# Performance work log

Hardware: AMD Instinct MI355X
Metric: run time of the kernel (lower is better)

The kernel has to match this reference:

```python
import jax, jax.numpy as jnp
import numpy as np

B, S, D, E, R, TOP_K = 4, 4096, 1024, 10, 4, 2
SCALING = 1.0 / R  # alpha / rank


def setup_inputs() -> dict:
    key = jax.random.key(0)
    ks = jax.random.split(key, 7)
    return {
        "x": jax.random.normal(ks[0], (B, S, D), dtype=jnp.float32),
        "W_base": jax.random.normal(ks[1], (D, D), dtype=jnp.float32) * (D ** -0.5),
        "b_base": jax.random.normal(ks[2], (D,), dtype=jnp.float32) * 0.02,
        "gate_W": jax.random.normal(ks[3], (E, D), dtype=jnp.float32) * (D ** -0.5),
        "gate_b": jax.random.normal(ks[4], (E,), dtype=jnp.float32) * 0.02,
        "lora_down": jax.random.normal(ks[5], (E, R, D), dtype=jnp.float32) * (D ** -0.5),
        "lora_up": jax.random.normal(ks[6], (E, D, R), dtype=jnp.float32) * (R ** -0.5),
    }


def reference(x, W_base, b_base, gate_W, gate_b, lora_down, lora_up):
    # Base (frozen) linear: [B,S,D]
    base_out = jnp.einsum("bsd,od->bso", x, W_base) + b_base

    # Top-k gating: logits [B,S,E] -> sparse softmax weights [B,S,E]
    logits = jnp.einsum("bsd,ed->bse", x, gate_W) + gate_b
    top_vals, top_idx = jax.lax.top_k(logits, TOP_K)          # [B,S,K]
    top_w = jax.nn.softmax(top_vals, axis=-1)                 # [B,S,K]
    # scatter top-k weights back to dense [B,S,E] (non-top-k are zero)
    weights = jnp.sum(top_w[..., None] * jax.nn.one_hot(top_idx, E, dtype=x.dtype), axis=-2)

    # All-expert LoRA (matches original loop); weight in rank space to avoid
    # materializing [B,S,E,D]: sum_e w_e * up_e(down_e(x)) * scaling
    h = jnp.einsum("bsd,erd->bser", x, lora_down)             # [B,S,E,R]
    h = h * weights[..., None]
    lora_out = jnp.einsum("bser,edr->bsd", h, lora_up) * SCALING

    return base_out + lora_out
```

## Files before the change

kernel.cpp:

```cpp
#include <hip/hip_runtime.h>
#include <hip/hip_bf16.h>
#include <cstdint>
#include <cstddef>

#define D_DIM 1024
#define E_NUM 10

typedef __attribute__((ext_vector_type(8))) short bf16x8;
typedef __attribute__((ext_vector_type(4))) float f32x4;
typedef unsigned short u16;
typedef unsigned int u32;

__device__ __forceinline__ u16 f2bf(float f) {
  union { float f; u32 u; } v; v.f = f;
  u32 r = v.u + 0x7fffu + ((v.u >> 16) & 1u);
  return (u16)(r >> 16);
}
__device__ __forceinline__ float bf2f(u16 u) {
  union { u32 u; float f; } v; v.u = ((u32)u) << 16; return v.f;
}
__device__ __forceinline__ float dot4(float4 a, float4 b) {
  return a.x * b.x + a.y * b.y + a.z * b.z + a.w * b.w;
}

__global__ void conv_w(const float* __restrict__ W, u16* __restrict__ Wb) {
  const int i = (blockIdx.x * 256 + threadIdx.x) * 8;
  float4 a = *(const float4*)(W + i);
  float4 b = *(const float4*)(W + i + 4);
  *(ushort4*)(Wb + i)     = make_ushort4(f2bf(a.x), f2bf(a.y), f2bf(a.z), f2bf(a.w));
  *(ushort4*)(Wb + i + 4) = make_ushort4(f2bf(b.x), f2bf(b.y), f2bf(b.z), f2bf(b.w));
}

__global__ void prep_ldb(const float* __restrict__ ld, u16* __restrict__ Bld) {
  const int r = blockIdx.x;
  for (int c = threadIdx.x; c < D_DIM; c += 256)
    Bld[r * D_DIM + c] = (r < 40) ? f2bf(ld[r * D_DIM + c]) : (u16)0;
}

__global__ __launch_bounds__(256)
void moe_prep_h(const float* __restrict__ x, const u16* __restrict__ Bld,
                float* __restrict__ h_all) {
  __shared__ u16 sX[4][16 * 64];
  __shared__ u16 sB[4][48 * 64];
  __shared__ float sP[4][3][16][17];

  const int tid = threadIdx.x, lane = tid & 63, w = tid >> 6;
  const int r0 = blockIdx.x * 16;
  const int kbase = w * 256;

  f32x4 acc[3] = {};

  float4 av[4];
#pragma unroll
  for (int i = 0; i < 2; ++i) {
    const int c = lane * 2 + i, row = c >> 3, kc = c & 7;
    const float* g = x + (size_t)(r0 + row) * D_DIM + kbase + kc * 8;
    av[i * 2]     = *(const float4*)g;
    av[i * 2 + 1] = *(const float4*)(g + 4);
  }

#pragma unroll 1
  for (int kt = 0; kt < 4; ++kt) {
    const int k0 = kbase + kt * 64;
#pragma unroll
    for (int i = 0; i < 6; ++i) {
      const int c = i * 64 + lane, row = c >> 3, kc = (c & 7) ^ (row & 7);
      __builtin_amdgcn_global_load_lds(
          (const __attribute__((address_space(1))) u32*)(Bld + (size_t)row * D_DIM + k0 + kc * 8),
          (__attribute__((address_space(3))) u32*)&sB[w][c * 8], 16, 0, 0);
    }
#pragma unroll
    for (int i = 0; i < 2; ++i) {
      const int c = lane * 2 + i, row = c >> 3, kc = c & 7;
      const float4 a = av[i * 2], b = av[i * 2 + 1];
      const int off = (row * 128 + kc * 16) ^ ((row & 7) << 4);
      *(ushort4*)((char*)sX[w] + off)     = make_ushort4(f2bf(a.x), f2bf(a.y), f2bf(a.z), f2bf(a.w));
      *(ushort4*)((char*)sX[w] + off + 8) = make_ushort4(f2bf(b.x), f2bf(b.y), f2bf(b.z), f2bf(b.w));
    }
    __syncthreads();
    if (kt < 3) {
#pragma unroll
      for (int i = 0; i < 2; ++i) {
        const int c = lane * 2 + i, row = c >> 3, kc = c & 7;
        const float* g = x + (size_t)(r0 + row) * D_DIM + (k0 + 64) + kc * 8;
        av[i * 2]     = *(const float4*)g;
        av[i * 2 + 1] = *(const float4*)(g + 4);
      }
    }
#pragma unroll
    for (int kk = 0; kk < 2; ++kk) {
      const int kb = kk * 64 + ((lane >> 4) * 16);
      const int rA = lane & 15;
      const bf16x8 a0 = *(const bf16x8*)((const char*)sX[w] + ((rA * 128 + kb) ^ ((rA & 7) << 4)));
#pragma unroll
      for (int cf = 0; cf < 3; ++cf) {
        const int rB = cf * 16 + (lane & 15);
        const bf16x8 q = *(const bf16x8*)((const char*)sB[w] + ((rB * 128 + kb) ^ ((rB & 7) << 4)));
        acc[cf] = __builtin_amdgcn_mfma_f32_16x16x32_bf16(a0, q, acc[cf], 0, 0, 0);
      }
    }
    __syncthreads();
  }

#pragma unroll
  for (int cf = 0; cf < 3; ++cf)
#pragma unroll
    for (int j = 0; j < 4; ++j)
      sP[w][cf][(lane >> 4) * 4 + j][lane & 15] = acc[cf][j];
  __syncthreads();

  const int row = tid >> 4, c16 = tid & 15;
#pragma unroll
  for (int cf = 0; cf < 3; ++cf) {
    const int col = cf * 16 + c16;
    if (col < 40) {
      const float s = sP[0][cf][row][c16] + sP[1][cf][row][c16] +
                      sP[2][cf][row][c16] + sP[3][cf][row][c16];
      h_all[(size_t)(r0 + row) * 40 + col] = s;
    }
  }
}

__global__ __launch_bounds__(256, 2)
void moe_gate(const float* __restrict__ x, const float* __restrict__ gW,
              const float* __restrict__ gb, const float* __restrict__ h_all,
              int* __restrict__ ids, float* __restrict__ cvals) {
  __shared__ float sgW[E_NUM * D_DIM];
  __shared__ float sgb[16];
  const int tid = threadIdx.x, lane = tid & 63, w = tid >> 6;
  for (int i = tid; i < E_NUM * D_DIM; i += 256) sgW[i] = gW[i];
  if (tid < E_NUM) sgb[tid] = gb[tid];
  __syncthreads();

  const int tb = blockIdx.x * 16 + w * 4;

  float4 xv[4][4];
#pragma unroll
  for (int tok = 0; tok < 4; ++tok)
#pragma unroll
    for (int j = 0; j < 4; ++j)
      xv[tok][j] = *(const float4*)(x + (size_t)(tb + tok) * D_DIM + j * 256 + lane * 4);

  float lg[4][E_NUM];
#pragma unroll
  for (int e = 0; e < E_NUM; ++e) {
    float a0 = 0.f, a1 = 0.f, a2 = 0.f, a3 = 0.f;
#pragma unroll
    for (int j = 0; j < 4; ++j) {
      const float4 wv = *(const float4*)(sgW + e * D_DIM + j * 256 + lane * 4);
      a0 += dot4(xv[0][j], wv);
      a1 += dot4(xv[1][j], wv);
      a2 += dot4(xv[2][j], wv);
      a3 += dot4(xv[3][j], wv);
    }
#pragma unroll
    for (int o = 32; o; o >>= 1) {
      a0 += __shfl_xor(a0, o);
      a1 += __shfl_xor(a1, o);
      a2 += __shfl_xor(a2, o);
      a3 += __shfl_xor(a3, o);
    }
    lg[0][e] = a0 + sgb[e];
    lg[1][e] = a1 + sgb[e];
    lg[2][e] = a2 + sgb[e];
    lg[3][e] = a3 + sgb[e];
  }

  if (lane < 4) {
    const int tok = lane, t = tb + tok;
    int e0 = 0; float v0 = lg[tok][0];
#pragma unroll
    for (int e = 1; e < E_NUM; ++e) if (lg[tok][e] > v0) { v0 = lg[tok][e]; e0 = e; }
    int e1 = -1; float v1 = -3.0e38f;
#pragma unroll
    for (int e = 0; e < E_NUM; ++e) if (e != e0 && lg[tok][e] > v1) { v1 = lg[tok][e]; e1 = e; }
    const float pp = expf(v1 - v0);
    const float inv = 1.f / (1.f + pp);
    const float s0 = inv * 0.25f, s1 = pp * inv * 0.25f;
    ids[t * 2] = e0; ids[t * 2 + 1] = e1;
    const float4 h0 = *(const float4*)(h_all + (size_t)t * 40 + e0 * 4);
    const float4 h1 = *(const float4*)(h_all + (size_t)t * 40 + e1 * 4);
    *(float4*)(cvals + t * 8)     = make_float4(h0.x * s0, h0.y * s0, h0.z * s0, h0.w * s0);
    *(float4*)(cvals + t * 8 + 4) = make_float4(h1.x * s1, h1.y * s1, h1.z * s1, h1.w * s1);
  }
}

__global__ __launch_bounds__(256, 2)
void moe_gemm_f32(const float* __restrict__ x, const u16* __restrict__ Wb,
                  const float* __restrict__ bias, const int* __restrict__ ids,
                  const float* __restrict__ cvals, const float* __restrict__ lup,
                  float* __restrict__ out) {
  __shared__ u16 Al[128 * 64];
  __shared__ u16 Bl[128 * 64];
  const int tid = threadIdx.x, lane = tid & 63, wid = tid >> 6;
  const int wm = wid >> 1, wn = wid & 1;
  const int p = blockIdx.x;
  const int cx = p & 7, q = p >> 3;
  const int nb = q & 7, mb = cx * 16 + (q >> 3);
  const int m0 = mb * 128, n0 = nb * 128;
  f32x4 acc[4][4] = {};
  float4 av[8];
#pragma unroll
  for (int t = 0; t < 8; ++t) {
    int c = t * 256 + tid, row = c >> 4, k4 = c & 15;
    av[t] = *(const float4*)(x + (size_t)(m0 + row) * D_DIM + k4 * 4);
  }
#pragma unroll 1
  for (int kt = 0; kt < 16; ++kt) {
    const int k0 = kt * 64;
#pragma unroll
    for (int i = 0; i < 4; ++i) {
      int c = i * 256 + tid, row = c >> 3, kc = (c & 7) ^ (row & 7);
      __builtin_amdgcn_global_load_lds(
          (const __attribute__((address_space(1))) u32*)(Wb + (size_t)(n0 + row) * D_DIM + k0 + kc * 8),
          (__attribute__((address_space(3))) u32*)&Bl[c * 8], 16, 0, 0);
    }
#pragma unroll
    for (int t = 0; t < 8; ++t) {
      int c = t * 256 + tid, row = c >> 4, k4 = c & 15;
      int off = (row * 128 + k4 * 8) ^ ((row & 7) << 4);
      *(ushort4*)((char*)Al + off) =
          make_ushort4(f2bf(av[t].x), f2bf(av[t].y), f2bf(av[t].z), f2bf(av[t].w));
    }
    __syncthreads();
    if (kt < 15) {
#pragma unroll
      for (int t = 0; t < 8; ++t) {
        int c = t * 256 + tid, row = c >> 4, k4 = c & 15;
        av[t] = *(const float4*)(x + (size_t)(m0 + row) * D_DIM + (k0 + 64) + k4 * 4);
      }
    }
#pragma unroll
    for (int kk = 0; kk < 2; ++kk) {
      bf16x8 af[4], bfr[4];
      const int kb = kk * 64 + ((lane >> 4) * 16);
#pragma unroll
      for (int m = 0; m < 4; ++m) {
        int row = wm * 64 + m * 16 + (lane & 15);
        af[m] = *(const bf16x8*)((const char*)Al + ((row * 128 + kb) ^ ((row & 7) << 4)));
      }
#pragma unroll
      for (int n = 0; n < 4; ++n) {
        int row = wn * 64 + n * 16 + (lane & 15);
        bfr[n] = *(const bf16x8*)((const char*)Bl + ((row * 128 + kb) ^ ((row & 7) << 4)));
      }
#pragma unroll
      for (int m = 0; m < 4; ++m)
#pragma unroll
        for (int n = 0; n < 4; ++n)
          acc[m][n] = __builtin_amdgcn_mfma_f32_16x16x32_bf16(af[m], bfr[n], acc[m][n], 0, 0, 0);
    }
    __syncthreads();
  }
  const int rg = lane >> 4, cl = lane & 15;
  const int baser = m0 + wm * 64, basec = n0 + wn * 64;
  float bs[4];
#pragma unroll
  for (int n = 0; n < 4; ++n) bs[n] = bias[basec + n * 16 + cl];
#pragma unroll
  for (int m = 0; m < 4; ++m)
#pragma unroll
    for (int j = 0; j < 4; ++j) {
      const int rr = baser + m * 16 + rg * 4 + j;
      const int2 id2 = *(const int2*)(ids + rr * 2);
      const float4 c0 = *(const float4*)(cvals + rr * 8);
      const float4 c1 = *(const float4*)(cvals + rr * 8 + 4);
      const float* u0b = lup + (size_t)id2.x * (D_DIM * 4);
      const float* u1b = lup + (size_t)id2.y * (D_DIM * 4);
#pragma unroll
      for (int n = 0; n < 4; ++n) {
        const int cc = basec + n * 16 + cl;
        float4 u0 = *(const float4*)(u0b + cc * 4);
        float4 u1 = *(const float4*)(u1b + cc * 4);
        float v = acc[m][n][j] + bs[n];
        v += c0.x * u0.x + c0.y * u0.y + c0.z * u0.z + c0.w * u0.w;
        v += c1.x * u1.x + c1.y * u1.y + c1.z * u1.z + c1.w * u1.w;
        out[(size_t)rr * D_DIM + cc] = v;
      }
    }
}

extern "C" void kernel_launch(void* const* d_in, const int* in_sizes, int n_in,
                              void* d_out, int out_size, void* d_ws, size_t ws_size,
                              hipStream_t stream) {
  const float* x   = (const float*)d_in[0];
  const float* Wb_ = (const float*)d_in[1];
  const float* bb  = (const float*)d_in[2];
  const float* gW  = (const float*)d_in[3];
  const float* gb  = (const float*)d_in[4];
  const float* ld  = (const float*)d_in[5];
  const float* lup = (const float*)d_in[6];

  char* w = (char*)d_ws;
  u16*   Wbf   = (u16*)w;
  u16*   Bld   = (u16*)(w + 2048ull * 1024);
  int*   ids   = (int*)(w + 2144ull * 1024);
  float* cvals = (float*)(w + 2272ull * 1024);
  float* h_all = (float*)(w + 2784ull * 1024);

  hipLaunchKernelGGL(conv_w,     dim3(512),  dim3(256), 0, stream, Wb_, Wbf);
  hipLaunchKernelGGL(prep_ldb,   dim3(48),   dim3(256), 0, stream, ld, Bld);
  hipLaunchKernelGGL(moe_prep_h, dim3(1024), dim3(256), 0, stream, x, Bld, h_all);
  hipLaunchKernelGGL(moe_gate,   dim3(1024), dim3(256), 0, stream, x, gW, gb, h_all, ids, cvals);
  hipLaunchKernelGGL(moe_gemm_f32, dim3(1024), dim3(256), 0, stream,
                     x, Wbf, bb, ids, cvals, lup, (float*)d_out);
}
```

Baseline: 130.7 us.

## Emit bf16 copy of x in prep kernel and run GEMM on bf16 A

The h-projection kernel already converts x to bf16, so it now also writes that bf16 copy to workspace. A new GEMM kernel reads bf16 A through direct global-to-LDS loads instead of re-reading fp32 x and converting it in registers. This halves the A-operand traffic and removes the conversion work from the main GEMM. The cost is an extra 32 MB write in the prep kernel, and the path only runs when the workspace is large enough.

```diff
diff --git a/kernel.cpp b/kernel.cpp
--- a/kernel.cpp
+++ b/kernel.cpp
@@ -39,7 +39,7 @@
 
 __global__ __launch_bounds__(256)
 void moe_prep_h(const float* __restrict__ x, const u16* __restrict__ Bld,
-                float* __restrict__ h_all) {
+                float* __restrict__ h_all, u16* __restrict__ xb) {
   __shared__ u16 sX[4][16 * 64];
   __shared__ u16 sB[4][48 * 64];
   __shared__ float sP[4][3][16][17];
@@ -73,9 +73,16 @@
     for (int i = 0; i < 2; ++i) {
       const int c = lane * 2 + i, row = c >> 3, kc = c & 7;
       const float4 a = av[i * 2], b = av[i * 2 + 1];
+      const ushort4 ha = make_ushort4(f2bf(a.x), f2bf(a.y), f2bf(a.z), f2bf(a.w));
+      const ushort4 hb = make_ushort4(f2bf(b.x), f2bf(b.y), f2bf(b.z), f2bf(b.w));
       const int off = (row * 128 + kc * 16) ^ ((row & 7) << 4);
-      *(ushort4*)((char*)sX[w] + off)     = make_ushort4(f2bf(a.x), f2bf(a.y), f2bf(a.z), f2bf(a.w));
-      *(ushort4*)((char*)sX[w] + off + 8) = make_ushort4(f2bf(b.x), f2bf(b.y), f2bf(b.z), f2bf(b.w));
+      *(ushort4*)((char*)sX[w] + off)     = ha;
+      *(ushort4*)((char*)sX[w] + off + 8) = hb;
+      if (xb) {
+        u16* dst = xb + (size_t)(r0 + row) * D_DIM + k0 + kc * 8;
+        *(ushort4*)dst       = ha;
+        *(ushort4*)(dst + 4) = hb;
+      }
     }
     __syncthreads();
     if (kt < 3) {
@@ -183,6 +190,92 @@
     *(float4*)(cvals + t * 8)     = make_float4(h0.x * s0, h0.y * s0, h0.z * s0, h0.w * s0);
     *(float4*)(cvals + t * 8 + 4) = make_float4(h1.x * s1, h1.y * s1, h1.z * s1, h1.w * s1);
   }
+}
+
+__global__ __launch_bounds__(256, 2)
+void moe_gemm_bf(const u16* __restrict__ xb, const u16* __restrict__ Wb,
+                 const float* __restrict__ bias, const int* __restrict__ ids,
+                 const float* __restrict__ cvals, const float* __restrict__ lup,
+                 float* __restrict__ out) {
+  __shared__ u16 Al[128 * 64];
+  __shared__ u16 Bl[128 * 64];
+
+  const int tid = threadIdx.x, lane = tid & 63, wid = tid >> 6;
+  const int wm = wid >> 1, wn = wid & 1;
+  const int p = blockIdx.x;
+  const int cx = p & 7, q = p >> 3;
+  const int nb = q & 7, mb = cx * 16 + (q >> 3);
+  const int m0 = mb * 128, n0 = nb * 128;
+
+  f32x4 acc[4][4] = {};
+
+#pragma unroll 1
+  for (int kt = 0; kt < 16; ++kt) {
+    const int k0 = kt * 64;
+#pragma unroll
+    for (int i = 0; i < 4; ++i) {
+      int c = i * 256 + tid, row = c >> 3, kc = (c & 7) ^ (row & 7);
+      __builtin_amdgcn_global_load_lds(
+          (const __attribute__((address_space(1))) u32*)(xb + (size_t)(m0 + row) * D_DIM + k0 + kc * 8),
+          (__attribute__((address_space(3))) u32*)&Al[c * 8], 16, 0, 0);
+    }
+#pragma unroll
+    for (int i = 0; i < 4; ++i) {
+      int c = i * 256 + tid, row = c >> 3, kc = (c & 7) ^ (row & 7);
+      __builtin_amdgcn_global_load_lds(
+          (const __attribute__((address_space(1))) u32*)(Wb + (size_t)(n0 + row) * D_DIM + k0 + kc * 8),
+          (__attribute__((address_space(3))) u32*)&Bl[c * 8], 16, 0, 0);
+    }
+    __syncthreads();
+#pragma unroll
+    for (int kk = 0; kk < 2; ++kk) {
+      bf16x8 af[4], bfr[4];
+      const int kb = kk * 64 + ((lane >> 4) * 16);
+#pragma unroll
+      for (int m = 0; m < 4; ++m) {
+        int row = wm * 64 + m * 16 + (lane & 15);
+        af[m] = *(const bf16x8*)((const char*)Al + ((row * 128 + kb) ^ ((row & 7) << 4)));
+      }
+#pragma unroll
+      for (int n = 0; n < 4; ++n) {
+        int row = wn * 64 + n * 16 + (lane & 15);
+        bfr[n] = *(const bf16x8*)((const char*)Bl + ((row * 128 + kb) ^ ((row & 7) << 4)));
+      }
+#pragma unroll
+      for (int m = 0; m < 4; ++m)
+#pragma unroll
+        for (int n = 0; n < 4; ++n)
+          acc[m][n] = __builtin_amdgcn_mfma_f32_16x16x32_bf16(af[m], bfr[n], acc[m][n], 0, 0, 0);
+    }
+    __syncthreads();
+  }
+
+  const int rg = lane >> 4, cl = lane & 15;
+  const int baser = m0 + wm * 64, basec = n0 + wn * 64;
+  float bs[4];
+#pragma unroll
+  for (int n = 0; n < 4; ++n) bs[n] = bias[basec + n * 16 + cl];
+#pragma unroll
+  for (int m = 0; m < 4; ++m)
+#pragma unroll
+    for (int j = 0; j < 4; ++j) {
+      const int rr = baser + m * 16 + rg * 4 + j;
+      const int2 id2 = *(const int2*)(ids + rr * 2);
+      const float4 c0 = *(const float4*)(cvals + rr * 8);
+      const float4 c1 = *(const float4*)(cvals + rr * 8 + 4);
+      const float* u0b = lup + (size_t)id2.x * (D_DIM * 4);
+      const float* u1b = lup + (size_t)id2.y * (D_DIM * 4);
+#pragma unroll
+      for (int n = 0; n < 4; ++n) {
+        const int cc = basec + n * 16 + cl;
+        float4 u0 = *(const float4*)(u0b + cc * 4);
+        float4 u1 = *(const float4*)(u1b + cc * 4);
+        float v = acc[m][n][j] + bs[n];
+        v += c0.x * u0.x + c0.y * u0.y + c0.z * u0.z + c0.w * u0.w;
+        v += c1.x * u1.x + c1.y * u1.y + c1.z * u1.z + c1.w * u1.w;
+        out[(size_t)rr * D_DIM + cc] = v;
+      }
+    }
 }
 
 __global__ __launch_bounds__(256, 2)
@@ -297,11 +390,18 @@
   int*   ids   = (int*)(w + 2144ull * 1024);
   float* cvals = (float*)(w + 2272ull * 1024);
   float* h_all = (float*)(w + 2784ull * 1024);
+  const size_t need_full = (5632ull + 32768ull) * 1024;
+  const bool full = ws_size >= need_full;
+  u16* xb = full ? (u16*)(w + 5632ull * 1024) : nullptr;
 
   hipLaunchKernelGGL(conv_w,     dim3(512),  dim3(256), 0, stream, Wb_, Wbf);
   hipLaunchKernelGGL(prep_ldb,   dim3(48),   dim3(256), 0, stream, ld, Bld);
-  hipLaunchKernelGGL(moe_prep_h, dim3(1024), dim3(256), 0, stream, x, Bld, h_all);
+  hipLaunchKernelGGL(moe_prep_h, dim3(1024), dim3(256), 0, stream, x, Bld, h_all, xb);
   hipLaunchKernelGGL(moe_gate,   dim3(1024), dim3(256), 0, stream, x, gW, gb, h_all, ids, cvals);
-  hipLaunchKernelGGL(moe_gemm_f32, dim3(1024), dim3(256), 0, stream,
-                     x, Wbf, bb, ids, cvals, lup, (float*)d_out);
-}
+  if (full)
+    hipLaunchKernelGGL(moe_gemm_bf, dim3(1024), dim3(256), 0, stream,
+                       xb, Wbf, bb, ids, cvals, lup, (float*)d_out);
+  else
+    hipLaunchKernelGGL(moe_gemm_f32, dim3(1024), dim3(256), 0, stream,
+                       x, Wbf, bb, ids, cvals, lup, (float*)d_out);
+}
```

After: 118.2 us. -9.6%, faster.

## Fold LoRA-up into GEMM as extra K tile with bf16 x and double-buffered loads

Applied to the files above, without the earlier changes.

moe_prep_h now also writes a bf16 copy of x, so the main GEMM streams bf16 A and B tiles directly into LDS via global_load_lds with double buffering, instead of converting fp32 x in registers. The LoRA up-projection is turned into a 17th K-tile: gate writes dense weighted rank activations (64-padded bf16) and a new prep kernel lays out lora_up as a bf16 [D,64] matrix, removing the scattered per-element epilogue gathers. The gate kernel reads gate weights from global memory instead of staging them in shared memory. The cost is an extra bf16 x write and read plus lower precision on the LoRA term.

```diff
diff --git a/kernel.cpp b/kernel.cpp
--- a/kernel.cpp
+++ b/kernel.cpp
@@ -37,9 +37,15 @@
     Bld[r * D_DIM + c] = (r < 40) ? f2bf(ld[r * D_DIM + c]) : (u16)0;
 }
 
+__global__ void prep_ub(const float* __restrict__ lup, u16* __restrict__ Ub) {
+  const int g = blockIdx.x * 256 + threadIdx.x;
+  const int o = g >> 6, j = g & 63;
+  Ub[g] = (j < 40) ? f2bf(lup[(size_t)(j >> 2) * (D_DIM * 4) + o * 4 + (j & 3)]) : (u16)0;
+}
+
 __global__ __launch_bounds__(256)
 void moe_prep_h(const float* __restrict__ x, const u16* __restrict__ Bld,
-                float* __restrict__ h_all) {
+                u16* __restrict__ hb, u16* __restrict__ xb) {
   __shared__ u16 sX[4][16 * 64];
   __shared__ u16 sB[4][48 * 64];
   __shared__ float sP[4][3][16][17];
@@ -73,9 +79,16 @@
     for (int i = 0; i < 2; ++i) {
       const int c = lane * 2 + i, row = c >> 3, kc = c & 7;
       const float4 a = av[i * 2], b = av[i * 2 + 1];
+      const ushort4 ha = make_ushort4(f2bf(a.x), f2bf(a.y), f2bf(a.z), f2bf(a.w));
+      const ushort4 hb4 = make_ushort4(f2bf(b.x), f2bf(b.y), f2bf(b.z), f2bf(b.w));
       const int off = (row * 128 + kc * 16) ^ ((row & 7) << 4);
-      *(ushort4*)((char*)sX[w] + off)     = make_ushort4(f2bf(a.x), f2bf(a.y), f2bf(a.z), f2bf(a.w));
-      *(ushort4*)((char*)sX[w] + off + 8) = make_ushort4(f2bf(b.x), f2bf(b.y), f2bf(b.z), f2bf(b.w));
+      *(ushort4*)((char*)sX[w] + off)     = ha;
+      *(ushort4*)((char*)sX[w] + off + 8) = hb4;
+      if (xb) {
+        u16* dst = xb + (size_t)(r0 + row) * D_DIM + k0 + kc * 8;
+        *(ushort4*)dst       = ha;
+        *(ushort4*)(dst + 4) = hb4;
+      }
     }
     __syncthreads();
     if (kt < 3) {
@@ -116,22 +129,16 @@
     if (col < 40) {
       const float s = sP[0][cf][row][c16] + sP[1][cf][row][c16] +
                       sP[2][cf][row][c16] + sP[3][cf][row][c16];
-      h_all[(size_t)(r0 + row) * 40 + col] = s;
+      hb[(size_t)(r0 + row) * 40 + col] = f2bf(s);
     }
   }
 }
 
 __global__ __launch_bounds__(256, 2)
 void moe_gate(const float* __restrict__ x, const float* __restrict__ gW,
-              const float* __restrict__ gb, const float* __restrict__ h_all,
-              int* __restrict__ ids, float* __restrict__ cvals) {
-  __shared__ float sgW[E_NUM * D_DIM];
-  __shared__ float sgb[16];
+              const float* __restrict__ gb, const u16* __restrict__ hb,
+              u16* __restrict__ cd) {
   const int tid = threadIdx.x, lane = tid & 63, w = tid >> 6;
-  for (int i = tid; i < E_NUM * D_DIM; i += 256) sgW[i] = gW[i];
-  if (tid < E_NUM) sgb[tid] = gb[tid];
-  __syncthreads();
-
   const int tb = blockIdx.x * 16 + w * 4;
 
   float4 xv[4][4];
@@ -147,7 +154,7 @@
     float a0 = 0.f, a1 = 0.f, a2 = 0.f, a3 = 0.f;
 #pragma unroll
     for (int j = 0; j < 4; ++j) {
-      const float4 wv = *(const float4*)(sgW + e * D_DIM + j * 256 + lane * 4);
+      const float4 wv = *(const float4*)(gW + e * D_DIM + j * 256 + lane * 4);
       a0 += dot4(xv[0][j], wv);
       a1 += dot4(xv[1][j], wv);
       a2 += dot4(xv[2][j], wv);
@@ -160,10 +167,11 @@
       a2 += __shfl_xor(a2, o);
       a3 += __shfl_xor(a3, o);
     }
-    lg[0][e] = a0 + sgb[e];
-    lg[1][e] = a1 + sgb[e];
-    lg[2][e] = a2 + sgb[e];
-    lg[3][e] = a3 + sgb[e];
+    const float be = gb[e];
+    lg[0][e] = a0 + be;
+    lg[1][e] = a1 + be;
+    lg[2][e] = a2 + be;
+    lg[3][e] = a3 + be;
   }
 
   if (lane < 4) {
@@ -177,72 +185,92 @@
     const float pp = expf(v1 - v0);
     const float inv = 1.f / (1.f + pp);
     const float s0 = inv * 0.25f, s1 = pp * inv * 0.25f;
-    ids[t * 2] = e0; ids[t * 2 + 1] = e1;
-    const float4 h0 = *(const float4*)(h_all + (size_t)t * 40 + e0 * 4);
-    const float4 h1 = *(const float4*)(h_all + (size_t)t * 40 + e1 * 4);
-    *(float4*)(cvals + t * 8)     = make_float4(h0.x * s0, h0.y * s0, h0.z * s0, h0.w * s0);
-    *(float4*)(cvals + t * 8 + 4) = make_float4(h1.x * s1, h1.y * s1, h1.z * s1, h1.w * s1);
+
+    u16* dst = cd + (size_t)t * 64;
+    const u16* hrow = hb + (size_t)t * 40;
+#pragma unroll
+    for (int e = 0; e < E_NUM; ++e) {
+      const float we = (e == e0) ? s0 : ((e == e1) ? s1 : 0.f);
+      const ushort4 hh = *(const ushort4*)(hrow + e * 4);
+      *(ushort4*)(dst + e * 4) = make_ushort4(
+          f2bf(bf2f(hh.x) * we), f2bf(bf2f(hh.y) * we),
+          f2bf(bf2f(hh.z) * we), f2bf(bf2f(hh.w) * we));
+    }
+#pragma unroll
+    for (int j = 40; j < 64; j += 4)
+      *(ushort4*)(dst + j) = make_ushort4(0, 0, 0, 0);
   }
 }
 
 __global__ __launch_bounds__(256, 2)
-void moe_gemm_f32(const float* __restrict__ x, const u16* __restrict__ Wb,
-                  const float* __restrict__ bias, const int* __restrict__ ids,
-                  const float* __restrict__ cvals, const float* __restrict__ lup,
-                  float* __restrict__ out) {
-  __shared__ u16 Al[128 * 64];
-  __shared__ u16 Bl[128 * 64];
+void moe_gemm_t(const u16* __restrict__ xb, const u16* __restrict__ Wbf,
+                const u16* __restrict__ cd, const u16* __restrict__ Ub,
+                const float* __restrict__ bias, float* __restrict__ out) {
+  __shared__ u16 Al[2][128 * 64];
+  __shared__ u16 Bl[2][128 * 64];
+
   const int tid = threadIdx.x, lane = tid & 63, wid = tid >> 6;
   const int wm = wid >> 1, wn = wid & 1;
   const int p = blockIdx.x;
   const int cx = p & 7, q = p >> 3;
   const int nb = q & 7, mb = cx * 16 + (q >> 3);
   const int m0 = mb * 128, n0 = nb * 128;
+
+  int sc_row[4], sc_kc[4];
+#pragma unroll
+  for (int i = 0; i < 4; ++i) {
+    const int c = i * 256 + tid;
+    sc_row[i] = c >> 3;
+    sc_kc[i]  = (c & 7) ^ (sc_row[i] & 7);
+  }
+
   f32x4 acc[4][4] = {};
-  float4 av[8];
-#pragma unroll
-  for (int t = 0; t < 8; ++t) {
-    int c = t * 256 + tid, row = c >> 4, k4 = c & 15;
-    av[t] = *(const float4*)(x + (size_t)(m0 + row) * D_DIM + k4 * 4);
-  }
+
+  auto STAGE = [&](int buf, int ktile) {
+    const u16* As; const u16* Bs; size_t str; int ko;
+    if (ktile < 16) {
+      As = xb + (size_t)m0 * D_DIM; Bs = Wbf + (size_t)n0 * D_DIM;
+      str = D_DIM; ko = ktile * 64;
+    } else {
+      As = cd + (size_t)m0 * 64; Bs = Ub + (size_t)n0 * 64;
+      str = 64; ko = 0;
+    }
+#pragma unroll
+    for (int i = 0; i < 4; ++i) {
+      const int c = i * 256 + tid;
+      __builtin_amdgcn_global_load_lds(
+          (const __attribute__((address_space(1))) u32*)(As + (size_t)sc_row[i] * str + ko + sc_kc[i] * 8),
+          (__attribute__((address_space(3))) u32*)&Al[buf][c * 8], 16, 0, 0);
+    }
+#pragma unroll
+    for (int i = 0; i < 4; ++i) {
+      const int c = i * 256 + tid;
+      __builtin_amdgcn_global_load_lds(
+          (const __attribute__((address_space(1))) u32*)(Bs + (size_t)sc_row[i] * str + ko + sc_kc[i] * 8),
+          (__attribute__((address_space(3))) u32*)&Bl[buf][c * 8], 16, 0, 0);
+    }
+  };
+
+  STAGE(0, 0);
+  __syncthreads();
+
 #pragma unroll 1
-  for (int kt = 0; kt < 16; ++kt) {
-    const int k0 = kt * 64;
-#pragma unroll
-    for (int i = 0; i < 4; ++i) {
-      int c = i * 256 + tid, row = c >> 3, kc = (c & 7) ^ (row & 7);
-      __builtin_amdgcn_global_load_lds(
-          (const __attribute__((address_space(1))) u32*)(Wb + (size_t)(n0 + row) * D_DIM + k0 + kc * 8),
-          (__attribute__((address_space(3))) u32*)&Bl[c * 8], 16, 0, 0);
-    }
-#pragma unroll
-    for (int t = 0; t < 8; ++t) {
-      int c = t * 256 + tid, row = c >> 4, k4 = c & 15;
-      int off = (row * 128 + k4 * 8) ^ ((row & 7) << 4);
-      *(ushort4*)((char*)Al + off) =
-          make_ushort4(f2bf(av[t].x), f2bf(av[t].y), f2bf(av[t].z), f2bf(av[t].w));
-    }
-    __syncthreads();
-    if (kt < 15) {
-#pragma unroll
-      for (int t = 0; t < 8; ++t) {
-        int c = t * 256 + tid, row = c >> 4, k4 = c & 15;
-        av[t] = *(const float4*)(x + (size_t)(m0 + row) * D_DIM + (k0 + 64) + k4 * 4);
-      }
-    }
+  for (int kt = 0; kt < 17; ++kt) {
+    const int cur = kt & 1;
+    if (kt < 16) STAGE(cur ^ 1, kt + 1);
 #pragma unroll
     for (int kk = 0; kk < 2; ++kk) {
       bf16x8 af[4], bfr[4];
       const int kb = kk * 64 + ((lane >> 4) * 16);
 #pragma unroll
       for (int m = 0; m < 4; ++m) {
-        int row = wm * 64 + m * 16 + (lane & 15);
-        af[m] = *(const bf16x8*)((const char*)Al + ((row * 128 + kb) ^ ((row & 7) << 4)));
+        const int row = wm * 64 + m * 16 + (lane & 15);
+        af[m] = *(const bf16x8*)((const char*)Al[cur] + ((row * 128 + kb) ^ ((row & 7) << 4)));
       }
 #pragma unroll
       for (int n = 0; n < 4; ++n) {
-        int row = wn * 64 + n * 16 + (lane & 15);
-        bfr[n] = *(const bf16x8*)((const char*)Bl + ((row * 128 + kb) ^ ((row & 7) << 4)));
+        const int row = wn * 64 + n * 16 + (lane & 15);
+        bfr[n] = *(const bf16x8*)((const char*)Bl[cur] + ((row * 128 + kb) ^ ((row & 7) << 4)));
       }
 #pragma unroll
       for (int m = 0; m < 4; ++m)
@@ -252,6 +280,7 @@
     }
     __syncthreads();
   }
+
   const int rg = lane >> 4, cl = lane & 15;
   const int baser = m0 + wm * 64, basec = n0 + wn * 64;
   float bs[4];
@@ -262,21 +291,9 @@
 #pragma unroll
     for (int j = 0; j < 4; ++j) {
       const int rr = baser + m * 16 + rg * 4 + j;
-      const int2 id2 = *(const int2*)(ids + rr * 2);
-      const float4 c0 = *(const float4*)(cvals + rr * 8);
-      const float4 c1 = *(const float4*)(cvals + rr * 8 + 4);
-      const float* u0b = lup + (size_t)id2.x * (D_DIM * 4);
-      const float* u1b = lup + (size_t)id2.y * (D_DIM * 4);
-#pragma unroll
-      for (int n = 0; n < 4; ++n) {
-        const int cc = basec + n * 16 + cl;
-        float4 u0 = *(const float4*)(u0b + cc * 4);
-        float4 u1 = *(const float4*)(u1b + cc * 4);
-        float v = acc[m][n][j] + bs[n];
-        v += c0.x * u0.x + c0.y * u0.y + c0.z * u0.z + c0.w * u0.w;
-        v += c1.x * u1.x + c1.y * u1.y + c1.z * u1.z + c1.w * u1.w;
-        out[(size_t)rr * D_DIM + cc] = v;
-      }
+#pragma unroll
+      for (int n = 0; n < 4; ++n)
+        out[(size_t)rr * D_DIM + basec + n * 16 + cl] = acc[m][n][j] + bs[n];
     }
 }
 
@@ -292,16 +309,18 @@
   const float* lup = (const float*)d_in[6];
 
   char* w = (char*)d_ws;
-  u16*   Wbf   = (u16*)w;
-  u16*   Bld   = (u16*)(w + 2048ull * 1024);
-  int*   ids   = (int*)(w + 2144ull * 1024);
-  float* cvals = (float*)(w + 2272ull * 1024);
-  float* h_all = (float*)(w + 2784ull * 1024);
+  u16* Wbf = (u16*)w;
+  u16* Ub  = (u16*)(w + 2048ull * 1024);
+  u16* Bld = (u16*)(w + 2176ull * 1024);
+  u16* cd  = (u16*)(w + 2272ull * 1024);
+  u16* hb  = (u16*)(w + 4320ull * 1024);
+  u16* xb  = (u16*)(w + 5600ull * 1024);
 
   hipLaunchKernelGGL(conv_w,     dim3(512),  dim3(256), 0, stream, Wb_, Wbf);
   hipLaunchKernelGGL(prep_ldb,   dim3(48),   dim3(256), 0, stream, ld, Bld);
-  hipLaunchKernelGGL(moe_prep_h, dim3(1024), dim3(256), 0, stream, x, Bld, h_all);
-  hipLaunchKernelGGL(moe_gate,   dim3(1024), dim3(256), 0, stream, x, gW, gb, h_all, ids, cvals);
-  hipLaunchKernelGGL(moe_gemm_f32, dim3(1024), dim3(256), 0, stream,
-                     x, Wbf, bb, ids, cvals, lup, (float*)d_out);
-}
+  hipLaunchKernelGGL(prep_ub,    dim3(256),  dim3(256), 0, stream, lup, Ub);
+  hipLaunchKernelGGL(moe_prep_h, dim3(1024), dim3(256), 0, stream, x, Bld, hb, xb);
+  hipLaunchKernelGGL(moe_gate,   dim3(1024), dim3(256), 0, stream, x, gW, gb, hb, cd);
+  hipLaunchKernelGGL(moe_gemm_t, dim3(1024), dim3(256), 0, stream,
+                     xb, Wbf, cd, Ub, bb, (float*)d_out);
+}
```

Result: faster. 119.3 us (-8.7%).
